# Performance work log

Measured on AMD Instinct MI355X. Metric: run time of the kernel, lower is better.

## Reference

```python
import jax, jax.numpy as jnp
import numpy as np

B, T, C, H = 2, 2048, 1024, 16
HS = C // H  # head_size = 64
EPS = 1e-5


def setup_inputs() -> dict:
    key = jax.random.key(0)
    ks = jax.random.split(key, 12)
    s = 0.02
    return {
        "x": jax.random.normal(ks[0], (B, T, C), jnp.float32),
        # per-head q/k/v linears stacked on a leading head axis [H, C, HS]
        "Wq": jax.random.normal(ks[1], (H, C, HS), jnp.float32) * s,
        "bq": jnp.zeros((H, HS), jnp.float32),
        "Wk": jax.random.normal(ks[2], (H, C, HS), jnp.float32) * s,
        "bk": jnp.zeros((H, HS), jnp.float32),
        "Wv": jax.random.normal(ks[3], (H, C, HS), jnp.float32) * s,
        "bv": jnp.zeros((H, HS), jnp.float32),
        # output projection [H*HS, C] == [C, C]
        "Wo": jax.random.normal(ks[4], (C, C), jnp.float32) * s,
        "bo": jnp.zeros((C,), jnp.float32),
        # feed-forward: C -> 4C -> C
        "W1": jax.random.normal(ks[5], (C, 4 * C), jnp.float32) * s,
        "b1": jnp.zeros((4 * C,), jnp.float32),
        "W2": jax.random.normal(ks[6], (4 * C, C), jnp.float32) * s,
        "b2": jnp.zeros((C,), jnp.float32),
        # custom LayerNorm params (broadcast over last dim)
        "gamma1": jnp.ones((C,), jnp.float32),
        "beta1": jnp.zeros((C,), jnp.float32),
        "gamma2": jnp.ones((C,), jnp.float32),
        "beta2": jnp.zeros((C,), jnp.float32),
    }


def _ln(x, gamma, beta):
    # NOTE: faithful to the source: normalizes over axis=1 (the SEQUENCE axis
    # for [B,T,C] input), uses unbiased variance (torch default), and puts eps
    # OUTSIDE the sqrt: (x - mean) / (sqrt(var) + eps).
    mean = x.mean(axis=1, keepdims=True)
    var = x.var(axis=1, keepdims=True, ddof=1)
    return gamma * ((x - mean) / (jnp.sqrt(var) + EPS)) + beta


def reference(x, Wq, bq, Wk, bk, Wv, bv, Wo, bo, W1, b1, W2, b2,
              gamma1, beta1, gamma2, beta2):
    # --- self-attention sublayer (pre-norm, residual) ---
    h = _ln(x, gamma1, beta1)
    q = jnp.einsum('btc,hcd->bhtd', h, Wq) + bq[None, :, None, :]
    k = jnp.einsum('btc,hcd->bhtd', h, Wk) + bk[None, :, None, :]
    v = jnp.einsum('btc,hcd->bhtd', h, Wv) + bv[None, :, None, :]
    wei = jax.nn.softmax(jnp.einsum('bhtd,bhsd->bhts', q, k) * (HS ** -0.5), axis=-1)
    attn = jnp.einsum('bhts,bhsd->bhtd', wei, v)          # [B,H,T,HS]
    attn = attn.transpose(0, 2, 1, 3).reshape(B, T, H * HS)  # head-order concat
    x = x + attn @ Wo + bo
    # --- feed-forward sublayer (pre-norm, residual) ---
    h2 = _ln(x, gamma2, beta2)
    x = x + jax.nn.relu(h2 @ W1 + b1) @ W2 + b2
    return x
```

## Files before the change

### kernel.cpp

```cpp
#include <hip/hip_runtime.h>
#include <hip/hip_bf16.h>

#define Bq 2
#define Tq 2048
#define Cq 1024
#define Hq 16
#define HSq 64
#define EPSq 1e-5f

using bf16 = __hip_bfloat16;
using f32x4 = __attribute__((ext_vector_type(4))) float;
using f32x16 = __attribute__((ext_vector_type(16))) float;
using bf16x8 = __attribute__((ext_vector_type(8))) __bf16;

__device__ __forceinline__ bf16 f2bf(float f) { return __float2bfloat16(f); }
__device__ __forceinline__ unsigned short f2u(float f) {
    return __builtin_bit_cast(unsigned short, __float2bfloat16(f));
}
__device__ __forceinline__ void gload16(const void* g, void* l) {
    __builtin_amdgcn_global_load_lds((const __attribute__((address_space(1))) void*)g,
                                     (__attribute__((address_space(3))) void*)l, 16, 0, 0);
}

__global__ void k_transpose(const float* __restrict__ src, bf16* __restrict__ dst,
                            int R, int Cc, long strideSrc, long strideDst) {
    __shared__ bf16 tile[32][33];
    const long zb = blockIdx.z;
    src += zb * strideSrc;
    dst += zb * strideDst;
    int c0 = blockIdx.x * 32, r0 = blockIdx.y * 32;
    int tx = threadIdx.x & 31, ty = threadIdx.x >> 5;
    for (int i = ty; i < 32; i += 8)
        tile[i][tx] = f2bf(src[(long)(r0 + i) * Cc + (c0 + tx)]);
    __syncthreads();
    for (int i = ty; i < 32; i += 8)
        dst[(long)(c0 + i) * R + (r0 + tx)] = tile[tx][i];
}

__global__ void k_transpose3(const float* __restrict__ Wq, const float* __restrict__ Wk,
                             const float* __restrict__ Wv, const float* __restrict__ bqv,
                             const float* __restrict__ bkv, const float* __restrict__ bvv,
                             bf16* __restrict__ dst, float* __restrict__ bdst) {
    __shared__ bf16 tile[32][33];
    const int zb = blockIdx.z;
    const int which = zb >> 4, head = zb & 15;
    const float* src = (which == 0 ? Wq : which == 1 ? Wk : Wv) + (long)head * 65536;
    bf16* d = dst + (long)which * 1048576 + (long)head * 65536;
    int c0 = blockIdx.x * 32, r0 = blockIdx.y * 32;
    int tx = threadIdx.x & 31, ty = threadIdx.x >> 5;
    for (int i = ty; i < 32; i += 8)
        tile[i][tx] = f2bf(src[(long)(r0 + i) * 64 + (c0 + tx)]);
    if (blockIdx.x == 0 && blockIdx.y == 0 && zb < 12) {
        int i = zb * 256 + threadIdx.x;
        bdst[i] = i < 1024 ? bqv[i] : i < 2048 ? bkv[i - 1024] : bvv[i - 2048];
    }
    __syncthreads();
    for (int i = ty; i < 32; i += 8)
        d[(long)(c0 + i) * 1024 + (r0 + tx)] = tile[tx][i];
}

__global__ void k_ln_part(const float* __restrict__ x, float* __restrict__ ps,
                          float* __restrict__ pss) {
    int c = blockIdx.x * 256 + threadIdx.x;
    int b = blockIdx.y;
    int tc = blockIdx.z;
    const float* p = x + (long)b * Tq * Cq + (long)tc * 64 * Cq + c;
    float s = 0.f, ss = 0.f;
    for (int t = 0; t < 64; ++t) {
        float v = p[(long)t * Cq];
        s += v;
        ss += v * v;
    }
    long o = ((long)tc * Bq + b) * Cq + c;
    ps[o] = s;
    pss[o] = ss;
}

__global__ void k_ln_fin(const float* __restrict__ ps, const float* __restrict__ pss,
                         float* __restrict__ mean, float* __restrict__ rstd) {
    int i = blockIdx.x * 256 + threadIdx.x;
    float s = 0.f, ss = 0.f;
    for (int tc = 0; tc < 32; ++tc) {
        s += ps[(long)tc * (Bq * Cq) + i];
        ss += pss[(long)tc * (Bq * Cq) + i];
    }
    float m = s / (float)Tq;
    float var = (ss - s * m) / (float)(Tq - 1);
    var = fmaxf(var, 0.f);
    mean[i] = m;
    rstd[i] = 1.0f / (sqrtf(var) + EPSq);
}

__global__ void k_ln_apply(const float* __restrict__ x, const float* __restrict__ mean,
                           const float* __restrict__ rstd, const float* __restrict__ gamma,
                           const float* __restrict__ beta, bf16* __restrict__ out) {
    long i = (long)blockIdx.x * 256 + threadIdx.x;
    int c = (int)(i & (Cq - 1));
    long bt = i >> 10;
    int b = (int)(bt >> 11);
    float m = mean[b * Cq + c], r = rstd[b * Cq + c];
    out[i] = f2bf(gamma[c] * ((x[i] - m) * r) + beta[c]);
}

__device__ __forceinline__ void xcd_swizzle(int& bx, int& by) {
    const int gx = gridDim.x;
    const int nwg = gx * gridDim.y;
    const int bid = blockIdx.y * gx + blockIdx.x;
    const int swz = (bid & 7) * (nwg >> 3) + (bid >> 3);
    bx = swz % gx;
    by = swz / gx;
}

template <int MODE>
__global__ __launch_bounds__(256, 3) void k_gemm_nt(
    const bf16* __restrict__ A, int lda, const bf16* __restrict__ Bt, int ldb, int K,
    const float* __restrict__ bias, bf16* __restrict__ outB, int ldout) {
    __shared__ __bf16 sA[2][128 * 32];
    __shared__ __bf16 sB[2][128 * 32];
    int bx, by;
    xcd_swizzle(bx, by);
    const int m0 = by * 128, n0 = bx * 128;
    const int tid = threadIdx.x;
    const int lane = tid & 63, wave = tid >> 6;
    const int lane15 = lane & 15, quad = lane >> 4;
    const int wm = (wave >> 1) * 64, wn = (wave & 1) * 64;
    const int srow = wave * 16 + (lane >> 2);
    const int scol = (((lane & 3) ^ ((lane >> 3) & 3)) * 8);
    const int sq8 = (quad ^ ((lane15 >> 1) & 3)) * 8;
    __bf16* a00 = &sA[0][wave * 512];
    __bf16* a01 = &sA[0][2048 + wave * 512];
    __bf16* a10 = &sA[1][wave * 512];
    __bf16* a11 = &sA[1][2048 + wave * 512];
    __bf16* b00 = &sB[0][wave * 512];
    __bf16* b01 = &sB[0][2048 + wave * 512];
    __bf16* b10 = &sB[1][wave * 512];
    __bf16* b11 = &sB[1][2048 + wave * 512];
    const bf16* Ap = A + (long)(m0 + srow) * lda + scol;
    const bf16* Ap2 = Ap + 64L * lda;
    const bf16* Bp = Bt + (long)(n0 + srow) * ldb + scol;
    const bf16* Bp2 = Bp + 64L * ldb;

    f32x4 acc[4][4];
#pragma unroll
    for (int i = 0; i < 4; ++i)
#pragma unroll
        for (int j = 0; j < 4; ++j)
#pragma unroll
            for (int p = 0; p < 4; ++p) acc[i][j][p] = 0.f;

    for (int k0 = 0; k0 < K; k0 += 64) {
        __syncthreads();
        gload16(Ap + k0, a00);
        gload16(Ap2 + k0, a01);
        gload16(Ap + k0 + 32, a10);
        gload16(Ap2 + k0 + 32, a11);
        gload16(Bp + k0, b00);
        gload16(Bp2 + k0, b01);
        gload16(Bp + k0 + 32, b10);
        gload16(Bp2 + k0 + 32, b11);
        __syncthreads();
#pragma unroll
        for (int kk = 0; kk < 2; ++kk) {
            bf16x8 af[4], bfr[4];
#pragma unroll
            for (int i = 0; i < 4; ++i)
                af[i] = *(const bf16x8*)(&sA[kk][(wm + i * 16 + lane15) * 32 + sq8]);
#pragma unroll
            for (int j = 0; j < 4; ++j)
                bfr[j] = *(const bf16x8*)(&sB[kk][(wn + j * 16 + lane15) * 32 + sq8]);
#pragma unroll
            for (int i = 0; i < 4; ++i)
#pragma unroll
                for (int j = 0; j < 4; ++j)
                    acc[i][j] = __builtin_amdgcn_mfma_f32_16x16x32_bf16(af[i], bfr[j],
                                                                        acc[i][j], 0, 0, 0);
        }
    }
    if (MODE == 0) {
#pragma unroll
        for (int i = 0; i < 4; ++i) {
            const int mm = m0 + wm + i * 16 + quad * 4;
            const int b = mm >> 11, t4 = mm & (Tq - 1);
#pragma unroll
            for (int j = 0; j < 4; ++j) {
                const int n = n0 + wn + j * 16 + lane15;
                const int which = n >> 10, hh = (n >> 6) & (Hq - 1), d = n & (HSq - 1);
                const long bh = (long)b * Hq + hh;
                const float bb = bias[n];
                if (which == 0) {
#pragma unroll
                    for (int p = 0; p < 4; ++p)
                        outB[bh * 131072 + (long)(t4 + p) * HSq + d] =
                            f2bf((acc[i][j][p] + bb) * 0.125f);
                } else if (which == 1) {
#pragma unroll
                    for (int p = 0; p < 4; ++p)
                        outB[4194304L + bh * 131072 + (long)(t4 + p) * HSq + d] =
                            f2bf(acc[i][j][p] + bb);
                } else {
                    ushort4 pk;
                    pk.x = f2u(acc[i][j][0] + bb);
                    pk.y = f2u(acc[i][j][1] + bb);
                    pk.z = f2u(acc[i][j][2] + bb);
                    pk.w = f2u(acc[i][j][3] + bb);
                    *(ushort4*)(&outB[8388608L + bh * 131072 + (long)d * Tq + t4]) = pk;
                }
            }
        }
    } else {
#pragma unroll
        for (int i = 0; i < 4; ++i) {
#pragma unroll
            for (int p = 0; p < 4; ++p) {
                const int m = m0 + wm + i * 16 + quad * 4 + p;
#pragma unroll
                for (int j = 0; j < 4; ++j) {
                    const int n = n0 + wn + j * 16 + lane15;
                    outB[(long)m * ldout + n] = f2bf(fmaxf(acc[i][j][p] + bias[n], 0.f));
                }
            }
        }
    }
}

template <int MODE>
__global__ __launch_bounds__(256, 2) void k_gemm_n64p(
    const bf16* __restrict__ A, int lda, const bf16* __restrict__ Bt, int ldb, int K,
    const float* __restrict__ bias, const float* __restrict__ residF,
    float* __restrict__ outF, int ldout) {
    __shared__ __bf16 lds[36864];
    int bx, by;
    xcd_swizzle(bx, by);
    const int m0 = by * 128, n0 = bx * 64;
    const int tid = threadIdx.x;
    const int lane = tid & 63, wave = tid >> 6;
    const int lane15 = lane & 15, quad = lane >> 4;
    const int wm = wave * 32;
    const int srow = wave * 16 + (lane >> 2);
    const int scol = (((lane & 3) ^ ((lane >> 3) & 3)) * 8);
    const int sq8 = (quad ^ ((lane15 >> 1) & 3)) * 8;
    const bf16* Ap = A + (long)(m0 + srow) * lda + scol;
    const bf16* Ap2 = Ap + 64L * lda;
    const bf16* Bp = Bt + (long)(n0 + srow) * ldb + scol;
    const int NT = K >> 6;

    f32x4 acc[2][4];
#pragma unroll
    for (int i = 0; i < 2; ++i)
#pragma unroll
        for (int j = 0; j < 4; ++j)
#pragma unroll
            for (int p = 0; p < 4; ++p) acc[i][j][p] = 0.f;

    auto stage = [&](int t, int ofs) {
        const long ko = (long)t << 6;
        __bf16* b = &lds[ofs + wave * 512];
        gload16(Ap + ko, b);
        gload16(Ap2 + ko, b + 2048);
        gload16(Ap + ko + 32, b + 4096);
        gload16(Ap2 + ko + 32, b + 6144);
        gload16(Bp + ko, b + 8192);
        gload16(Bp + ko + 32, b + 10240);
    };
    auto comp = [&](int ofs) {
        const __bf16* base = &lds[ofs];
#pragma unroll
        for (int kk = 0; kk < 2; ++kk) {
            bf16x8 af[2], bfr[4];
#pragma unroll
            for (int i = 0; i < 2; ++i)
                af[i] = *(const bf16x8*)(base + kk * 4096 + (wm + i * 16 + lane15) * 32 + sq8);
#pragma unroll
            for (int j = 0; j < 4; ++j)
                bfr[j] =
                    *(const bf16x8*)(base + 8192 + kk * 2048 + (j * 16 + lane15) * 32 + sq8);
#pragma unroll
            for (int i = 0; i < 2; ++i)
#pragma unroll
                for (int j = 0; j < 4; ++j)
                    acc[i][j] = __builtin_amdgcn_mfma_f32_16x16x32_bf16(af[i], bfr[j],
                                                                        acc[i][j], 0, 0, 0);
        }
    };

    stage(0, 0);
    stage(1, 12288);
    int o0 = 0, o1 = 12288, o2 = 24576;
    for (int t = 0; t < NT - 1; ++t) {
        asm volatile("s_waitcnt vmcnt(6)" ::: "memory");
        __builtin_amdgcn_s_barrier();
        if (t + 2 < NT) stage(t + 2, o2);
        comp(o0);
        const int tmp = o0;
        o0 = o1;
        o1 = o2;
        o2 = tmp;
    }
    asm volatile("s_waitcnt vmcnt(0)" ::: "memory");
    __builtin_amdgcn_s_barrier();
    comp(o0);

#pragma unroll
    for (int i = 0; i < 2; ++i) {
#pragma unroll
        for (int p = 0; p < 4; ++p) {
            const int m = m0 + wm + i * 16 + quad * 4 + p;
#pragma unroll
            for (int j = 0; j < 4; ++j) {
                const int n = n0 + j * 16 + lane15;
                outF[(long)m * ldout + n] =
                    acc[i][j][p] + bias[n] + residF[(long)m * ldout + n];
            }
        }
    }
}

__global__ __launch_bounds__(512, 2) void k_gemm_8ph(
    const bf16* __restrict__ A, int lda, const bf16* __restrict__ Bt, int ldb, int K,
    const float* __restrict__ bias, bf16* __restrict__ outB, int ldout) {
    __shared__ __bf16 sA[2][2][256 * 32];
    __shared__ __bf16 sB[2][2][256 * 32];
    int bx, by;
    xcd_swizzle(bx, by);
    const int m0 = by * 256, n0 = bx * 256;
    const int tid = threadIdx.x;
    const int lane = tid & 63, wave = tid >> 6;
    const int lane15 = lane & 15, quad = lane >> 4;
    const int wr = wave >> 2, wc = wave & 3;
    const int sq8 = (quad ^ ((lane15 >> 1) & 3)) * 8;
    const int arow = wr * 128 + lane15;
    const int brow = wc * 64 + lane15;
    const int sr = wave * 16 + (lane >> 2);
    const int sc = ((lane & 3) ^ ((lane >> 3) & 3)) * 8;
    const bf16* ApS = A + (long)(m0 + sr) * lda + sc;
    const bf16* BpS = Bt + (long)(n0 + sr) * ldb + sc;
    const int NT = K >> 6;
    const int NP = NT << 2;

    auto stage_plane = [&](int q) {
        if (q >= NP) return;
        const int t = q >> 2, slot = q & 3;
        const int db = t & 1, kk = slot >> 1;
        const long ko = ((long)t << 6) + kk * 32;
        if (!(slot & 1)) {
            gload16(ApS + ko, &sA[db][kk][wave * 512]);
            gload16(ApS + ko + 128L * lda, &sA[db][kk][4096 + wave * 512]);
        } else {
            gload16(BpS + ko, &sB[db][kk][wave * 512]);
            gload16(BpS + ko + 128L * ldb, &sB[db][kk][4096 + wave * 512]);
        }
    };

    f32x4 acc[8][4];
#pragma unroll
    for (int i = 0; i < 8; ++i)
#pragma unroll
        for (int j = 0; j < 4; ++j)
#pragma unroll
            for (int p = 0; p < 4; ++p) acc[i][j][p] = 0.f;

    stage_plane(0);
    stage_plane(1);
    stage_plane(2);
    stage_plane(3);
    stage_plane(4);
    stage_plane(5);
    asm volatile("s_waitcnt vmcnt(4)" ::: "memory");
    __builtin_amdgcn_s_barrier();

    for (int t = 0; t < NT; ++t) {
        const int db = t & 1;
        const __bf16* A0 = sA[db][0];
        const __bf16* A1 = sA[db][1];
        const __bf16* B0 = sB[db][0];
        const __bf16* B1 = sB[db][1];
        bf16x8 af[4], bfx[4];
#pragma unroll
        for (int j = 0; j < 4; ++j)
            bfx[j] = *(const bf16x8*)(&B0[(brow + j * 16) * 32 + sq8]);
#pragma unroll
        for (int ii = 0; ii < 4; ++ii)
            af[ii] = *(const bf16x8*)(&A0[(arow + ii * 16) * 32 + sq8]);
        stage_plane(4 * t + 6);
        __builtin_amdgcn_s_barrier();
        __builtin_amdgcn_s_setprio(1);
#pragma unroll
        for (int ii = 0; ii < 4; ++ii)
#pragma unroll
            for (int j = 0; j < 4; ++j)
                acc[ii][j] =
                    __builtin_amdgcn_mfma_f32_16x16x32_bf16(af[ii], bfx[j], acc[ii][j], 0, 0, 0);
        __builtin_amdgcn_s_setprio(0);
        __builtin_amdgcn_s_barrier();
#pragma unroll
        for (int ii = 0; ii < 4; ++ii)
            af[ii] = *(const bf16x8*)(&A0[(arow + 64 + ii * 16) * 32 + sq8]);
        stage_plane(4 * t + 7);
        __builtin_amdgcn_s_barrier();
        __builtin_amdgcn_s_setprio(1);
#pragma unroll
        for (int ii = 0; ii < 4; ++ii)
#pragma unroll
            for (int j = 0; j < 4; ++j)
                acc[4 + ii][j] = __builtin_amdgcn_mfma_f32_16x16x32_bf16(af[ii], bfx[j],
                                                                         acc[4 + ii][j], 0, 0, 0);
        __builtin_amdgcn_s_setprio(0);
        __builtin_amdgcn_s_barrier();
#pragma unroll
        for (int j = 0; j < 4; ++j)
            bfx[j] = *(const bf16x8*)(&B1[(brow + j * 16) * 32 + sq8]);
#pragma unroll
        for (int ii = 0; ii < 4; ++ii)
            af[ii] = *(const bf16x8*)(&A1[(arow + ii * 16) * 32 + sq8]);
        stage_plane(4 * t + 8);
        __builtin_amdgcn_s_barrier();
        __builtin_amdgcn_s_setprio(1);
#pragma unroll
        for (int ii = 0; ii < 4; ++ii)
#pragma unroll
            for (int j = 0; j < 4; ++j)
                acc[ii][j] =
                    __builtin_amdgcn_mfma_f32_16x16x32_bf16(af[ii], bfx[j], acc[ii][j], 0, 0, 0);
        __builtin_amdgcn_s_setprio(0);
        __builtin_amdgcn_s_barrier();
#pragma unroll
        for (int ii = 0; ii < 4; ++ii)
            af[ii] = *(const bf16x8*)(&A1[(arow + 64 + ii * 16) * 32 + sq8]);
        stage_plane(4 * t + 9);
        __builtin_amdgcn_s_barrier();
        __builtin_amdgcn_s_setprio(1);
#pragma unroll
        for (int ii = 0; ii < 4; ++ii)
#pragma unroll
            for (int j = 0; j < 4; ++j)
                acc[4 + ii][j] = __builtin_amdgcn_mfma_f32_16x16x32_bf16(af[ii], bfx[j],
                                                                         acc[4 + ii][j], 0, 0, 0);
        __builtin_amdgcn_s_setprio(0);
        asm volatile("s_waitcnt vmcnt(4)" ::: "memory");
        __builtin_amdgcn_s_barrier();
    }
#pragma unroll
    for (int i = 0; i < 8; ++i) {
#pragma unroll
        for (int p = 0; p < 4; ++p) {
            const int m = m0 + wr * 128 + i * 16 + quad * 4 + p;
#pragma unroll
            for (int j = 0; j < 4; ++j) {
                const int n = n0 + wc * 64 + j * 16 + lane15;
                outB[(long)m * ldout + n] = f2bf(fmaxf(acc[i][j][p] + bias[n], 0.f));
            }
        }
    }
}

__global__ __launch_bounds__(256, 4) void k_attn(const bf16* __restrict__ qkv,
                                                 float* __restrict__ po0,
                                                 float* __restrict__ po1,
                                                 float* __restrict__ rs0,
                                                 float* __restrict__ rs1) {
    __shared__ __bf16 sK[64 * 72];
    __shared__ __bf16 sVt[64 * 72];
    const int bh = blockIdx.y;
    const int q0 = blockIdx.x * 128;
    const int z = blockIdx.z;
    const int kc0 = z << 10;
    float* __restrict__ po = z ? po1 : po0;
    float* __restrict__ rsb = z ? rs1 : rs0;
    const int tid = threadIdx.x, wave = tid >> 6, lane = tid & 63;
    const int lane31 = lane & 31, laneh = lane >> 5;
    const bf16* Qp = qkv + (long)bh * 131072;
    const bf16* Kp = qkv + 4194304L + (long)bh * 131072;
    const bf16* Vtp = qkv + 8388608L + (long)bh * 131072;
    bf16x8 qa[4];
#pragma unroll
    for (int s = 0; s < 4; ++s)
        qa[s] = *(const bf16x8*)(&Qp[(long)(q0 + wave * 32 + lane31) * HSq + s * 16 + laneh * 8]);
    f32x16 o[2];
#pragma unroll
    for (int dt = 0; dt < 2; ++dt)
#pragma unroll
        for (int r = 0; r < 16; ++r) o[dt][r] = 0.f;
    float rs = 0.f;
    const int r0 = tid >> 3, c0 = (tid & 7) * 8;
    const int r1 = r0 + 32;

    uint4 nk0 = *(const uint4*)(&Kp[(long)(kc0 + r0) * HSq + c0]);
    uint4 nk1 = *(const uint4*)(&Kp[(long)(kc0 + r1) * HSq + c0]);
    uint4 nv0 = *(const uint4*)(&Vtp[(long)r0 * Tq + kc0 + c0]);
    uint4 nv1 = *(const uint4*)(&Vtp[(long)r1 * Tq + kc0 + c0]);

    for (int kc = kc0; kc < kc0 + 1024; kc += 64) {
        __syncthreads();
        *(uint4*)(&sK[r0 * 72 + c0]) = nk0;
        *(uint4*)(&sK[r1 * 72 + c0]) = nk1;
        *(uint4*)(&sVt[r0 * 72 + c0]) = nv0;
        *(uint4*)(&sVt[r1 * 72 + c0]) = nv1;
        __syncthreads();
        if (kc + 64 < kc0 + 1024) {
            nk0 = *(const uint4*)(&Kp[(long)(kc + 64 + r0) * HSq + c0]);
            nk1 = *(const uint4*)(&Kp[(long)(kc + 64 + r1) * HSq + c0]);
            nv0 = *(const uint4*)(&Vtp[(long)r0 * Tq + kc + 64 + c0]);
            nv1 = *(const uint4*)(&Vtp[(long)r1 * Tq + kc + 64 + c0]);
        }
#pragma unroll
        for (int nt = 0; nt < 2; ++nt) {
            f32x16 zz;
#pragma unroll
            for (int r = 0; r < 16; ++r) zz[r] = 0.f;
            __builtin_amdgcn_s_setprio(1);
#pragma unroll
            for (int s = 0; s < 4; ++s) {
                bf16x8 kb =
                    *(const bf16x8*)(&sK[(nt * 32 + lane31) * 72 + s * 16 + laneh * 8]);
                zz = __builtin_amdgcn_mfma_f32_32x32x16_bf16(kb, qa[s], zz, 0, 0, 0);
            }
            __builtin_amdgcn_s_setprio(0);
            float e[16];
#pragma unroll
            for (int r = 0; r < 16; ++r) {
                e[r] = __expf(zz[r]);
                rs += e[r];
            }
            unsigned int pk[8];
#pragma unroll
            for (int g = 0; g < 4; ++g)
#pragma unroll
                for (int h = 0; h < 2; ++h)
                    pk[g * 2 + h] = (unsigned int)f2u(e[g * 4 + 2 * h]) |
                                    ((unsigned int)f2u(e[g * 4 + 2 * h + 1]) << 16);
            unsigned int sa0 = laneh ? pk[0] : pk[2], sa1 = laneh ? pk[1] : pk[3];
            unsigned int ra0 = __shfl_xor((int)sa0, 32), ra1 = __shfl_xor((int)sa1, 32);
            unsigned int sb0 = laneh ? pk[4] : pk[6], sb1 = laneh ? pk[5] : pk[7];
            unsigned int rb0 = __shfl_xor((int)sb0, 32), rb1 = __shfl_xor((int)sb1, 32);
            uint4 f0, f1;
            if (laneh == 0) {
                f0 = {pk[0], pk[1], ra0, ra1};
                f1 = {pk[4], pk[5], rb0, rb1};
            } else {
                f0 = {ra0, ra1, pk[2], pk[3]};
                f1 = {rb0, rb1, pk[6], pk[7]};
            }
            bf16x8 pa0 = __builtin_bit_cast(bf16x8, f0);
            bf16x8 pa1 = __builtin_bit_cast(bf16x8, f1);
            __builtin_amdgcn_s_setprio(1);
#pragma unroll
            for (int dt = 0; dt < 2; ++dt) {
                bf16x8 vb0 =
                    *(const bf16x8*)(&sVt[(dt * 32 + lane31) * 72 + nt * 32 + laneh * 8]);
                bf16x8 vb1 = *(const bf16x8*)(&sVt[(dt * 32 + lane31) * 72 + nt * 32 + 16 +
                                                   laneh * 8]);
                o[dt] = __builtin_amdgcn_mfma_f32_32x32x16_bf16(pa0, vb0, o[dt], 0, 0, 0);
                o[dt] = __builtin_amdgcn_mfma_f32_32x32x16_bf16(pa1, vb1, o[dt], 0, 0, 0);
            }
            __builtin_amdgcn_s_setprio(0);
        }
    }
    float ltot = rs + __shfl_xor(rs, 32);
    if (laneh == 0) rsb[(bh << 11) + q0 + wave * 32 + lane31] = ltot;
#pragma unroll
    for (int r = 0; r < 16; ++r) {
        const int tl = (r & 3) + 8 * (r >> 2) + 4 * laneh;
        const int t = q0 + wave * 32 + tl;
        float* pb = po + ((long)(bh << 11) + t) * 64;
#pragma unroll
        for (int dt = 0; dt < 2; ++dt) pb[dt * 32 + lane31] = o[dt][r];
    }
}

__global__ __launch_bounds__(256) void k_attn_combine(
    const float* __restrict__ po0, const float* __restrict__ po1,
    const float* __restrict__ rs0, const float* __restrict__ rs1,
    bf16* __restrict__ out) {
    const long i = ((long)blockIdx.x * 256 + threadIdx.x) * 4;
    const int d = (int)(i & 63);
    const long qq = i >> 6;
    const int bh = (int)(qq >> 11), t = (int)(qq & 2047);
    const float inv = 1.0f / (rs0[qq] + rs1[qq]);
    const f32x4 a = *(const f32x4*)(po0 + i);
    const f32x4 b = *(const f32x4*)(po1 + i);
    const int bb = bh >> 4, hh = bh & 15;
    ushort4 pk;
    pk.x = f2u((a[0] + b[0]) * inv);
    pk.y = f2u((a[1] + b[1]) * inv);
    pk.z = f2u((a[2] + b[2]) * inv);
    pk.w = f2u((a[3] + b[3]) * inv);
    *(ushort4*)(&out[(((long)bb * Tq + t) << 10) + hh * 64 + d]) = pk;
}

extern "C" void kernel_launch(void* const* d_in, const int* in_sizes, int n_in,
                              void* d_out, int out_size, void* d_ws, size_t ws_size,
                              hipStream_t stream) {
    const float* x = (const float*)d_in[0];
    const float* Wq = (const float*)d_in[1];
    const float* bqv = (const float*)d_in[2];
    const float* Wk = (const float*)d_in[3];
    const float* bkv = (const float*)d_in[4];
    const float* Wv = (const float*)d_in[5];
    const float* bvv = (const float*)d_in[6];
    const float* Wo = (const float*)d_in[7];
    const float* bo = (const float*)d_in[8];
    const float* W1 = (const float*)d_in[9];
    const float* b1 = (const float*)d_in[10];
    const float* W2 = (const float*)d_in[11];
    const float* b2 = (const float*)d_in[12];
    const float* g1 = (const float*)d_in[13];
    const float* be1 = (const float*)d_in[14];
    const float* g2 = (const float*)d_in[15];
    const float* be2 = (const float*)d_in[16];

    char* ws = (char*)d_ws;
    size_t off = 0;
    auto alloc = [&](size_t bytes) {
        void* p = ws + off;
        off += (bytes + 255) & ~(size_t)255;
        return p;
    };
    bf16* regA = (bf16*)alloc(32L * 1024 * 1024);
    float* x2 = (float*)alloc(4096L * 1024 * 4);
    bf16* buf1 = (bf16*)alloc(4096L * 1024 * 2);
    float* bqkv = (float*)alloc(3072L * 4);
    float* ps = (float*)alloc(32L * Bq * Cq * 4);
    float* pss = (float*)alloc(32L * Bq * Cq * 4);
    float* mean1 = (float*)alloc(Bq * Cq * 4);
    float* rstd1 = (float*)alloc(Bq * Cq * 4);
    float* mean2 = (float*)alloc(Bq * Cq * 4);
    float* rstd2 = (float*)alloc(Bq * Cq * 4);
    bf16* dres = (bf16*)d_out;
    float* outF = (float*)d_out;
    float* po1 = (float*)d_out;
    bf16* attn_out = regA + 12582912;

    k_ln_part<<<dim3(4, Bq, 32), 256, 0, stream>>>(x, ps, pss);
    k_ln_fin<<<dim3(8), 256, 0, stream>>>(ps, pss, mean1, rstd1);
    k_ln_apply<<<dim3(16384), 256, 0, stream>>>(x, mean1, rstd1, g1, be1, dres);

    k_transpose3<<<dim3(2, 32, 48), 256, 0, stream>>>(Wq, Wk, Wv, bqv, bkv, bvv, buf1, bqkv);
    k_gemm_nt<0><<<dim3(24, 32), 256, 0, stream>>>(dres, 1024, buf1, 1024, 1024, bqkv, regA, 0);
    k_attn<<<dim3(16, 32, 2), 256, 0, stream>>>(regA, x2, po1, ps, pss);
    k_attn_combine<<<dim3(4096), 256, 0, stream>>>(x2, po1, ps, pss, attn_out);
    k_transpose<<<dim3(32, 32, 1), 256, 0, stream>>>(Wo, buf1, 1024, 1024, 0, 0);
    k_gemm_n64p<1><<<dim3(16, 32), 256, 0, stream>>>(attn_out, 1024, buf1, 1024, 1024, bo, x,
                                                     x2, 1024);
    k_ln_part<<<dim3(4, Bq, 32), 256, 0, stream>>>(x2, ps, pss);
    k_ln_fin<<<dim3(8), 256, 0, stream>>>(ps, pss, mean2, rstd2);
    k_ln_apply<<<dim3(16384), 256, 0, stream>>>(x2, mean2, rstd2, g2, be2, dres);

    k_transpose<<<dim3(128, 32, 1), 256, 0, stream>>>(W1, buf1, 1024, 4096, 0, 0);
    k_gemm_8ph<<<dim3(16, 16), 512, 0, stream>>>(dres, 1024, buf1, 1024, 1024, b1, regA, 4096);
    k_transpose<<<dim3(32, 128, 1), 256, 0, stream>>>(W2, buf1, 4096, 1024, 0, 0);
    k_gemm_n64p<3><<<dim3(16, 32), 256, 0, stream>>>(regA, 4096, buf1, 4096, 4096, b2, x2,
                                                     outF, 1024);
}
```

Baseline: 369.2 us.

## Route QKV projection through 8-phase GEMM, remap attention blocks per XCD, use exp2

The QKV projection now runs on the larger-tile 8-phase 512-thread GEMM instead of the 128x128 kernel, which is removed. Its epilogue writes the Q/K/V head layouts directly and folds log2(e) into the Q scale, so attention can call exp2f instead of __expf. Attention blocks are remapped so each XCD handles a contiguous group of (batch, head) pairs, aiming to keep K/V in the local L2. The tradeoff is a coarser grid for the QKV GEMM (192 blocks), which may leave some CUs idle.

```diff
diff --git a/kernel.cpp b/kernel.cpp
--- a/kernel.cpp
+++ b/kernel.cpp
@@ -21,6 +21,8 @@
     __builtin_amdgcn_global_load_lds((const __attribute__((address_space(1))) void*)g,
                                      (__attribute__((address_space(3))) void*)l, 16, 0, 0);
 }
+
+#define QSCALE 0.180336884f
 
 __global__ void k_transpose(const float* __restrict__ src, bf16* __restrict__ dst,
                             int R, int Cc, long strideSrc, long strideDst) {
@@ -109,118 +111,6 @@
     const int swz = (bid & 7) * (nwg >> 3) + (bid >> 3);
     bx = swz % gx;
     by = swz / gx;
-}
-
-template <int MODE>
-__global__ __launch_bounds__(256, 3) void k_gemm_nt(
-    const bf16* __restrict__ A, int lda, const bf16* __restrict__ Bt, int ldb, int K,
-    const float* __restrict__ bias, bf16* __restrict__ outB, int ldout) {
-    __shared__ __bf16 sA[2][128 * 32];
-    __shared__ __bf16 sB[2][128 * 32];
-    int bx, by;
-    xcd_swizzle(bx, by);
-    const int m0 = by * 128, n0 = bx * 128;
-    const int tid = threadIdx.x;
-    const int lane = tid & 63, wave = tid >> 6;
-    const int lane15 = lane & 15, quad = lane >> 4;
-    const int wm = (wave >> 1) * 64, wn = (wave & 1) * 64;
-    const int srow = wave * 16 + (lane >> 2);
-    const int scol = (((lane & 3) ^ ((lane >> 3) & 3)) * 8);
-    const int sq8 = (quad ^ ((lane15 >> 1) & 3)) * 8;
-    __bf16* a00 = &sA[0][wave * 512];
-    __bf16* a01 = &sA[0][2048 + wave * 512];
-    __bf16* a10 = &sA[1][wave * 512];
-    __bf16* a11 = &sA[1][2048 + wave * 512];
-    __bf16* b00 = &sB[0][wave * 512];
-    __bf16* b01 = &sB[0][2048 + wave * 512];
-    __bf16* b10 = &sB[1][wave * 512];
-    __bf16* b11 = &sB[1][2048 + wave * 512];
-    const bf16* Ap = A + (long)(m0 + srow) * lda + scol;
-    const bf16* Ap2 = Ap + 64L * lda;
-    const bf16* Bp = Bt + (long)(n0 + srow) * ldb + scol;
-    const bf16* Bp2 = Bp + 64L * ldb;
-
-    f32x4 acc[4][4];
-#pragma unroll
-    for (int i = 0; i < 4; ++i)
-#pragma unroll
-        for (int j = 0; j < 4; ++j)
-#pragma unroll
-            for (int p = 0; p < 4; ++p) acc[i][j][p] = 0.f;
-
-    for (int k0 = 0; k0 < K; k0 += 64) {
-        __syncthreads();
-        gload16(Ap + k0, a00);
-        gload16(Ap2 + k0, a01);
-        gload16(Ap + k0 + 32, a10);
-        gload16(Ap2 + k0 + 32, a11);
-        gload16(Bp + k0, b00);
-        gload16(Bp2 + k0, b01);
-        gload16(Bp + k0 + 32, b10);
-        gload16(Bp2 + k0 + 32, b11);
-        __syncthreads();
-#pragma unroll
-        for (int kk = 0; kk < 2; ++kk) {
-            bf16x8 af[4], bfr[4];
-#pragma unroll
-            for (int i = 0; i < 4; ++i)
-                af[i] = *(const bf16x8*)(&sA[kk][(wm + i * 16 + lane15) * 32 + sq8]);
-#pragma unroll
-            for (int j = 0; j < 4; ++j)
-                bfr[j] = *(const bf16x8*)(&sB[kk][(wn + j * 16 + lane15) * 32 + sq8]);
-#pragma unroll
-            for (int i = 0; i < 4; ++i)
-#pragma unroll
-                for (int j = 0; j < 4; ++j)
-                    acc[i][j] = __builtin_amdgcn_mfma_f32_16x16x32_bf16(af[i], bfr[j],
-                                                                        acc[i][j], 0, 0, 0);
-        }
-    }
-    if (MODE == 0) {
-#pragma unroll
-        for (int i = 0; i < 4; ++i) {
-            const int mm = m0 + wm + i * 16 + quad * 4;
-            const int b = mm >> 11, t4 = mm & (Tq - 1);
-#pragma unroll
-            for (int j = 0; j < 4; ++j) {
-                const int n = n0 + wn + j * 16 + lane15;
-                const int which = n >> 10, hh = (n >> 6) & (Hq - 1), d = n & (HSq - 1);
-                const long bh = (long)b * Hq + hh;
-                const float bb = bias[n];
-                if (which == 0) {
-#pragma unroll
-                    for (int p = 0; p < 4; ++p)
-                        outB[bh * 131072 + (long)(t4 + p) * HSq + d] =
-                            f2bf((acc[i][j][p] + bb) * 0.125f);
-                } else if (which == 1) {
-#pragma unroll
-                    for (int p = 0; p < 4; ++p)
-                        outB[4194304L + bh * 131072 + (long)(t4 + p) * HSq + d] =
-                            f2bf(acc[i][j][p] + bb);
-                } else {
-                    ushort4 pk;
-                    pk.x = f2u(acc[i][j][0] + bb);
-                    pk.y = f2u(acc[i][j][1] + bb);
-                    pk.z = f2u(acc[i][j][2] + bb);
-                    pk.w = f2u(acc[i][j][3] + bb);
-                    *(ushort4*)(&outB[8388608L + bh * 131072 + (long)d * Tq + t4]) = pk;
-                }
-            }
-        }
-    } else {
-#pragma unroll
-        for (int i = 0; i < 4; ++i) {
-#pragma unroll
-            for (int p = 0; p < 4; ++p) {
-                const int m = m0 + wm + i * 16 + quad * 4 + p;
-#pragma unroll
-                for (int j = 0; j < 4; ++j) {
-                    const int n = n0 + wn + j * 16 + lane15;
-                    outB[(long)m * ldout + n] = f2bf(fmaxf(acc[i][j][p] + bias[n], 0.f));
-                }
-            }
-        }
-    }
 }
 
 template <int MODE>
@@ -315,6 +205,7 @@
     }
 }
 
+template <int MODE>
 __global__ __launch_bounds__(512, 2) void k_gemm_8ph(
     const bf16* __restrict__ A, int lda, const bf16* __restrict__ Bt, int ldb, int K,
     const float* __restrict__ bias, bf16* __restrict__ outB, int ldout) {
@@ -439,15 +330,48 @@
         asm volatile("s_waitcnt vmcnt(4)" ::: "memory");
         __builtin_amdgcn_s_barrier();
     }
-#pragma unroll
-    for (int i = 0; i < 8; ++i) {
-#pragma unroll
-        for (int p = 0; p < 4; ++p) {
-            const int m = m0 + wr * 128 + i * 16 + quad * 4 + p;
+    if (MODE == 0) {
+#pragma unroll
+        for (int i = 0; i < 8; ++i) {
+            const int mm = m0 + wr * 128 + i * 16 + quad * 4;
+            const int b = mm >> 11, t4 = mm & (Tq - 1);
 #pragma unroll
             for (int j = 0; j < 4; ++j) {
                 const int n = n0 + wc * 64 + j * 16 + lane15;
-                outB[(long)m * ldout + n] = f2bf(fmaxf(acc[i][j][p] + bias[n], 0.f));
+                const int which = n >> 10, hh = (n >> 6) & (Hq - 1), d = n & (HSq - 1);
+                const long bh = (long)b * Hq + hh;
+                const float bb = bias[n];
+                if (which == 0) {
+#pragma unroll
+                    for (int p = 0; p < 4; ++p)
+                        outB[bh * 131072 + (long)(t4 + p) * HSq + d] =
+                            f2bf((acc[i][j][p] + bb) * QSCALE);
+                } else if (which == 1) {
+#pragma unroll
+                    for (int p = 0; p < 4; ++p)
+                        outB[4194304L + bh * 131072 + (long)(t4 + p) * HSq + d] =
+                            f2bf(acc[i][j][p] + bb);
+                } else {
+                    ushort4 pk;
+                    pk.x = f2u(acc[i][j][0] + bb);
+                    pk.y = f2u(acc[i][j][1] + bb);
+                    pk.z = f2u(acc[i][j][2] + bb);
+                    pk.w = f2u(acc[i][j][3] + bb);
+                    *(ushort4*)(&outB[8388608L + bh * 131072 + (long)d * Tq + t4]) = pk;
+                }
+            }
+        }
+    } else {
+#pragma unroll
+        for (int i = 0; i < 8; ++i) {
+#pragma unroll
+            for (int p = 0; p < 4; ++p) {
+                const int m = m0 + wr * 128 + i * 16 + quad * 4 + p;
+#pragma unroll
+                for (int j = 0; j < 4; ++j) {
+                    const int n = n0 + wc * 64 + j * 16 + lane15;
+                    outB[(long)m * ldout + n] = f2bf(fmaxf(acc[i][j][p] + bias[n], 0.f));
+                }
             }
         }
     }
@@ -460,9 +384,12 @@
                                                  float* __restrict__ rs1) {
     __shared__ __bf16 sK[64 * 72];
     __shared__ __bf16 sVt[64 * 72];
-    const int bh = blockIdx.y;
-    const int q0 = blockIdx.x * 128;
-    const int z = blockIdx.z;
+    const int nlin = blockIdx.x + (int)(gridDim.x * (blockIdx.y + gridDim.y * blockIdx.z));
+    const int xcd = nlin & 7, s = nlin >> 3;
+    const int bh = (xcd << 2) | (s >> 5);
+    const int rem = s & 31;
+    const int q0 = (rem & 15) * 128;
+    const int z = rem >> 4;
     const int kc0 = z << 10;
     float* __restrict__ po = z ? po1 : po0;
     float* __restrict__ rsb = z ? rs1 : rs0;
@@ -473,8 +400,8 @@
     const bf16* Vtp = qkv + 8388608L + (long)bh * 131072;
     bf16x8 qa[4];
 #pragma unroll
-    for (int s = 0; s < 4; ++s)
-        qa[s] = *(const bf16x8*)(&Qp[(long)(q0 + wave * 32 + lane31) * HSq + s * 16 + laneh * 8]);
+    for (int s2 = 0; s2 < 4; ++s2)
+        qa[s2] = *(const bf16x8*)(&Qp[(long)(q0 + wave * 32 + lane31) * HSq + s2 * 16 + laneh * 8]);
     f32x16 o[2];
 #pragma unroll
     for (int dt = 0; dt < 2; ++dt)
@@ -509,16 +436,16 @@
             for (int r = 0; r < 16; ++r) zz[r] = 0.f;
             __builtin_amdgcn_s_setprio(1);
 #pragma unroll
-            for (int s = 0; s < 4; ++s) {
+            for (int s2 = 0; s2 < 4; ++s2) {
                 bf16x8 kb =
-                    *(const bf16x8*)(&sK[(nt * 32 + lane31) * 72 + s * 16 + laneh * 8]);
-                zz = __builtin_amdgcn_mfma_f32_32x32x16_bf16(kb, qa[s], zz, 0, 0, 0);
+                    *(const bf16x8*)(&sK[(nt * 32 + lane31) * 72 + s2 * 16 + laneh * 8]);
+                zz = __builtin_amdgcn_mfma_f32_32x32x16_bf16(kb, qa[s2], zz, 0, 0, 0);
             }
             __builtin_amdgcn_s_setprio(0);
             float e[16];
 #pragma unroll
             for (int r = 0; r < 16; ++r) {
-                e[r] = __expf(zz[r]);
+                e[r] = exp2f(zz[r]);
                 rs += e[r];
             }
             unsigned int pk[8];
@@ -635,7 +562,7 @@
     k_ln_apply<<<dim3(16384), 256, 0, stream>>>(x, mean1, rstd1, g1, be1, dres);
 
     k_transpose3<<<dim3(2, 32, 48), 256, 0, stream>>>(Wq, Wk, Wv, bqv, bkv, bvv, buf1, bqkv);
-    k_gemm_nt<0><<<dim3(24, 32), 256, 0, stream>>>(dres, 1024, buf1, 1024, 1024, bqkv, regA, 0);
+    k_gemm_8ph<0><<<dim3(12, 16), 512, 0, stream>>>(dres, 1024, buf1, 1024, 1024, bqkv, regA, 0);
     k_attn<<<dim3(16, 32, 2), 256, 0, stream>>>(regA, x2, po1, ps, pss);
     k_attn_combine<<<dim3(4096), 256, 0, stream>>>(x2, po1, ps, pss, attn_out);
     k_transpose<<<dim3(32, 32, 1), 256, 0, stream>>>(Wo, buf1, 1024, 1024, 0, 0);
@@ -646,7 +573,8 @@
     k_ln_apply<<<dim3(16384), 256, 0, stream>>>(x2, mean2, rstd2, g2, be2, dres);
 
     k_transpose<<<dim3(128, 32, 1), 256, 0, stream>>>(W1, buf1, 1024, 4096, 0, 0);
-    k_gemm_8ph<<<dim3(16, 16), 512, 0, stream>>>(dres, 1024, buf1, 1024, 1024, b1, regA, 4096);
+    k_gemm_8ph<2><<<dim3(16, 16), 512, 0, stream>>>(dres, 1024, buf1, 1024, 1024, b1, regA,
+                                                    4096);
     k_transpose<<<dim3(32, 128, 1), 256, 0, stream>>>(W2, buf1, 4096, 1024, 0, 0);
     k_gemm_n64p<3><<<dim3(16, 32), 256, 0, stream>>>(regA, 4096, buf1, 4096, 4096, b2, x2,
                                                      outF, 1024);
```

Measured after the change: 389.0 us. +5.4%, slower.
